# Optimization experiments

Measured on AMD Instinct MI355X. Metric: run time of the kernel, lower is better.

The kernel has to match this reference:

```python
import jax, jax.numpy as jnp
import numpy as np
import math

POOL = 7          # RoIAlign output_size
SR = 2            # sampling_ratio


def _roi_align(feat, boxes, bidx):
    """torchvision RoIAlign, aligned=False, spatial_scale=1.0, sampling_ratio=2.
    feat: [B,C,H,W]; boxes: [N,4] (x1,y1,x2,y2) in pixel coords of this level;
    bidx: [N] int batch indices. Returns [N,C,POOL,POOL]."""
    B, C, H, W = feat.shape
    x1, y1, x2, y2 = boxes[:, 0], boxes[:, 1], boxes[:, 2], boxes[:, 3]
    roi_w = jnp.maximum(x2 - x1, 1.0)
    roi_h = jnp.maximum(y2 - y1, 1.0)
    bin_w = roi_w / POOL
    bin_h = roi_h / POOL
    # sample-point offsets within the ROI, in bin units: [POOL, SR]
    off = jnp.arange(POOL, dtype=feat.dtype)[:, None] + (jnp.arange(SR, dtype=feat.dtype)[None, :] + 0.5) / SR
    ys = y1[:, None, None] + bin_h[:, None, None] * off  # [N,POOL,SR]
    xs = x1[:, None, None] + bin_w[:, None, None] * off  # [N,POOL,SR]

    def prep(c, size):
        valid = (c > -1.0) & (c < size)
        c = jnp.clip(c, 0.0, size - 1)
        lo = jnp.floor(c).astype(jnp.int32)
        hi = jnp.minimum(lo + 1, size - 1)
        return lo, hi, c - lo, valid

    y_lo, y_hi, fy, vy = prep(ys, H)
    x_lo, x_hi, fx, vx = prep(xs, W)

    b = bidx.astype(jnp.int32)[:, None, None, None, None]  # [N,1,1,1,1]

    def gather(yi, xi):
        # -> [N,POOL,SR,POOL,SR,C] (advanced indices broadcast, channel slice last)
        return feat[b, :, yi[:, :, :, None, None], xi[:, None, None, :, :]]

    hy = (1.0 - fy)[:, :, :, None, None, None]
    ly = fy[:, :, :, None, None, None]
    hx = (1.0 - fx)[:, None, None, :, :, None]
    lx = fx[:, None, None, :, :, None]
    v = (gather(y_lo, x_lo) * hy * hx + gather(y_lo, x_hi) * hy * lx
         + gather(y_hi, x_lo) * ly * hx + gather(y_hi, x_hi) * ly * lx)
    valid = (vy[:, :, :, None, None] & vx[:, None, None, :, :])[..., None]
    v = jnp.where(valid, v, 0.0)
    out = v.mean(axis=(2, 4))          # average over SRxSR samples -> [N,POOL,POOL,C]
    return out.transpose(0, 3, 1, 2)   # [N,C,POOL,POOL]


def setup_inputs() -> dict:
    key = jax.random.key(0)
    k2, k3, k4, k5, kxy, kwh, kbi = jax.random.split(key, 7)
    N = 1000
    p2 = jax.random.normal(k2, (2, 256, 256, 256), dtype=jnp.float32)
    p3 = jax.random.normal(k3, (2, 256, 128, 128), dtype=jnp.float32)
    p4 = jax.random.normal(k4, (2, 256, 64, 64), dtype=jnp.float32)
    p5 = jax.random.normal(k5, (2, 256, 32, 32), dtype=jnp.float32)
    xy = jax.random.uniform(kxy, (N, 2), minval=0.0, maxval=0.7)
    wh = jax.random.uniform(kwh, (N, 2), minval=0.02, maxval=0.3)
    rpn_bbox = jnp.concatenate([xy, xy + wh], axis=1)  # (x1,y1,x2,y2) normalized
    box_index = jax.random.randint(kbi, (N,), 0, 2, dtype=jnp.int32)
    return {"p2": p2, "p3": p3, "p4": p4, "p5": p5,
            "rpn_bbox": rpn_bbox, "box_index": box_index}


def reference(p2, p3, p4, p5, rpn_bbox, box_index):
    feats = [p2, p3, p4, p5]
    N = rpn_bbox.shape[0]
    x1, y1, x2, y2 = rpn_bbox[:, 0], rpn_bbox[:, 1], rpn_bbox[:, 2], rpn_bbox[:, 3]
    area = (y2 - y1) * (x2 - x1)
    roi_level = jnp.log(jnp.sqrt(area)) / math.log(2.0)
    roi_level = jnp.clip(jnp.round(roi_level) + 4.0, 0.0, 3.0).astype(jnp.int32)
    # Compute RoIAlign of every ROI at every level, then select per-ROI level.
    # (The masked-select / per-level dispatch / argsort-combine in the original
    # restores original ROI order, so this is mathematically identical.)
    pooled_per_level = jnp.stack(
        [_roi_align(f, rpn_bbox * f.shape[3], box_index) for f in feats], axis=0
    )  # [4, N, C, 7, 7]
    pooled = pooled_per_level[roi_level, jnp.arange(N)]  # [N, C, 7, 7]
    return pooled
```

## Files before the change

### kernel.cpp

```cpp
#include <hip/hip_runtime.h>
#include <math.h>

#define POOL 7
#define NCELL 49
#define NCH 256
#define CH_SPLIT 4
#define CHPB (NCH / CH_SPLIT)
#define CHPW (CHPB / 4)
#define LDSF 640
#define NIT 10

__global__ __launch_bounds__(256) void roi_align_fpn_kernel(
    const float* __restrict__ p2, const float* __restrict__ p3,
    const float* __restrict__ p4, const float* __restrict__ p5,
    const float* __restrict__ boxes, const int* __restrict__ bidx,
    float* __restrict__ out, int N)
{
    __shared__ float smem[4][LDSF];
    const int n = blockIdx.x;
    if (n >= N) return;
    const int t = threadIdx.x;
    const int wave = t >> 6;
    const int lane = t & 63;

    float bx1 = boxes[4 * n + 0], by1 = boxes[4 * n + 1];
    float bx2 = boxes[4 * n + 2], by2 = boxes[4 * n + 3];
    float area = (by2 - by1) * (bx2 - bx1);
    float lvlf = logf(sqrtf(area)) * 1.4426950408889634f;
    int level = (int)fminf(fmaxf(rintf(lvlf) + 4.0f, 0.0f), 3.0f);
    int W = 256 >> level;
    int HW = W * W;
    float scale = (float)W;
    float x1 = bx1 * scale, y1 = by1 * scale;
    float bin_w = fmaxf((bx2 - bx1) * scale, 1.0f) * (1.0f / POOL);
    float bin_h = fmaxf((by2 - by1) * scale, 1.0f) * (1.0f / POOL);

    const float* feat = (level == 0) ? p2 : (level == 1) ? p3 : (level == 2) ? p4 : p5;
    feat += (size_t)bidx[n] * NCH * HW;

    float yA = y1 + bin_h * 0.25f, yB = y1 + bin_h * 6.75f;
    float xA = x1 + bin_w * 0.25f, xB = x1 + bin_w * 6.75f;
    int y0  = (int)floorf(fminf(fmaxf(yA, 0.f), (float)(W - 1)));
    int y1h = min((int)floorf(fminf(fmaxf(yB, 0.f), (float)(W - 1))) + 1, W - 1);
    int x0  = (int)floorf(fminf(fmaxf(xA, 0.f), (float)(W - 1)));
    x0 = min(x0, W - 2);
    int x1p = min((int)floorf(fminf(fmaxf(xB, 0.f), (float)(W - 1))) + 1, W - 1);
    int ww = x1p - x0 + 1;
    int wh = y1h - y0 + 1;
    wh = min(wh, LDSF / ww);
    int packed = ww * wh;

    int g_off[NIT];
#pragma unroll
    for (int k = 0; k < NIT; ++k) {
        int idx = k * 64 + lane;
        idx = (idx < packed) ? idx : 0;
        int r = idx / ww;
        int c = idx - r * ww;
        g_off[k] = (y0 + r) * W + (x0 + c);
    }

    int cell = (lane < NCELL) ? lane : (NCELL - 1);
    int py = cell / POOL, px = cell % POOL;
    int loff0[4], loff1[4];
    float w00[4], w01[4], w10[4], w11[4];
#pragma unroll
    for (int s = 0; s < 4; ++s) {
        int sy = s >> 1, sx = s & 1;
        float y = y1 + bin_h * ((float)py + ((float)sy + 0.5f) * 0.5f);
        float x = x1 + bin_w * ((float)px + ((float)sx + 0.5f) * 0.5f);
        bool v = (y > -1.f) && (y < (float)W) && (x > -1.f) && (x < (float)W);
        float yc = fminf(fmaxf(y, 0.f), (float)(W - 1));
        float xc = fminf(fmaxf(x, 0.f), (float)(W - 1));
        int ylo = (int)floorf(yc), xlo = (int)floorf(xc);
        int yhi = min(ylo + 1, W - 1);
        float fy = yc - (float)ylo, fx = xc - (float)xlo;
        float vv = v ? 0.25f : 0.f;
        int bxp = min(xlo, W - 2);
        bool in = (xlo == bxp);
        float wx0 = in ? (1.f - fx) : 0.f;
        float wx1 = in ? fx : 1.f;
        float wr0 = (1.f - fy) * vv, wr1 = fy * vv;
        loff0[s] = (ylo - y0) * ww + (bxp - x0);
        loff1[s] = (yhi - y0) * ww + (bxp - x0);
        w00[s] = wr0 * wx0; w01[s] = wr0 * wx1;
        w10[s] = wr1 * wx0; w11[s] = wr1 * wx1;
    }

    float* sm = smem[wave];
    const int ch0 = blockIdx.y * CHPB + wave * CHPW;
    const float* f = feat + (size_t)ch0 * HW;
    size_t obase = (size_t)n * NCH * NCELL + (size_t)ch0 * NCELL + cell;
#pragma unroll 2
    for (int i = 0; i < CHPW; ++i) {
        const float* fc = f + (size_t)i * HW;
        float g[NIT];
#pragma unroll
        for (int k = 0; k < NIT; ++k) g[k] = fc[g_off[k]];
#pragma unroll
        for (int k = 0; k < NIT; ++k) sm[k * 64 + lane] = g[k];
        float acc = 0.f;
#pragma unroll
        for (int s = 0; s < 4; ++s) {
            float a0 = sm[loff0[s]], a1 = sm[loff0[s] + 1];
            float b0 = sm[loff1[s]], b1 = sm[loff1[s] + 1];
            acc += w00[s] * a0 + w01[s] * a1 + w10[s] * b0 + w11[s] * b1;
        }
        if (lane < NCELL)
            __builtin_nontemporal_store(acc, out + obase + (size_t)i * NCELL);
    }
}

extern "C" void kernel_launch(void* const* d_in, const int* in_sizes, int n_in,
                              void* d_out, int out_size, void* d_ws, size_t ws_size,
                              hipStream_t stream) {
    const float* p2    = (const float*)d_in[0];
    const float* p3    = (const float*)d_in[1];
    const float* p4    = (const float*)d_in[2];
    const float* p5    = (const float*)d_in[3];
    const float* boxes = (const float*)d_in[4];
    const int*   bidx  = (const int*)d_in[5];
    float* out = (float*)d_out;
    int N = in_sizes[5];
    dim3 grid(N, CH_SPLIT);
    roi_align_fpn_kernel<<<grid, 256, 0, stream>>>(p2, p3, p4, p5, boxes, bidx, out, N);
}
```

Measured before the change: 286.3 us.

## Double-buffer feature patches via async global-to-LDS loads and reorder grid

Replaces register-staged gathers with global_load_lds async copies into a double-buffered per-wave LDS region, prefetching the next channel's patch while the current one is interpolated. It doubles the channel split and swaps the grid axes so that blocks for the same ROI launch adjacently, which should improve L2 locality, and it raises the launch-bounds occupancy hint. The goal is to hide gather latency and cut register traffic. In exchange it relies on manual vmcnt waits, doubles LDS use per block, and drops the N bounds check.

```diff
diff --git a/kernel.cpp b/kernel.cpp
--- a/kernel.cpp
+++ b/kernel.cpp
@@ -4,21 +4,26 @@
 #define POOL 7
 #define NCELL 49
 #define NCH 256
-#define CH_SPLIT 4
+#define CH_SPLIT 8
 #define CHPB (NCH / CH_SPLIT)
 #define CHPW (CHPB / 4)
 #define LDSF 640
 #define NIT 10
 
-__global__ __launch_bounds__(256) void roi_align_fpn_kernel(
+typedef __attribute__((address_space(1))) void global_void;
+typedef __attribute__((address_space(3))) void lds_void;
+__device__ __forceinline__ void async_stage(const float* g, float* l) {
+    __builtin_amdgcn_global_load_lds((global_void*)g, (lds_void*)l, 4, 0, 0);
+}
+
+__global__ __launch_bounds__(256, 8) void roi_align_fpn_kernel(
     const float* __restrict__ p2, const float* __restrict__ p3,
     const float* __restrict__ p4, const float* __restrict__ p5,
     const float* __restrict__ boxes, const int* __restrict__ bidx,
     float* __restrict__ out, int N)
 {
-    __shared__ float smem[4][LDSF];
-    const int n = blockIdx.x;
-    if (n >= N) return;
+    __shared__ float smem[4][2][LDSF];
+    const int n = blockIdx.y;
     const int t = threadIdx.x;
     const int wave = t >> 6;
     const int lane = t & 63;
@@ -60,6 +65,13 @@
         g_off[k] = (y0 + r) * W + (x0 + c);
     }
 
+    const int ch0 = blockIdx.x * CHPB + wave * CHPW;
+    const float* fbase = feat + (size_t)ch0 * HW;
+    float* sm = &smem[wave][0][0];
+
+#pragma unroll
+    for (int k = 0; k < NIT; ++k) async_stage(fbase + g_off[k], sm + k * 64);
+
     int cell = (lane < NCELL) ? lane : (NCELL - 1);
     int py = cell / POOL, px = cell % POOL;
     int loff0[4], loff1[4];
@@ -87,23 +99,24 @@
         w10[s] = wr1 * wx0; w11[s] = wr1 * wx1;
     }
 
-    float* sm = smem[wave];
-    const int ch0 = blockIdx.y * CHPB + wave * CHPW;
-    const float* f = feat + (size_t)ch0 * HW;
     size_t obase = (size_t)n * NCH * NCELL + (size_t)ch0 * NCELL + cell;
-#pragma unroll 2
+#pragma unroll
     for (int i = 0; i < CHPW; ++i) {
-        const float* fc = f + (size_t)i * HW;
-        float g[NIT];
+        if (i + 1 < CHPW) {
+            const float* fc = fbase + (size_t)(i + 1) * HW;
+            float* nb = sm + ((i + 1) & 1) * LDSF;
 #pragma unroll
-        for (int k = 0; k < NIT; ++k) g[k] = fc[g_off[k]];
-#pragma unroll
-        for (int k = 0; k < NIT; ++k) sm[k * 64 + lane] = g[k];
+            for (int k = 0; k < NIT; ++k) async_stage(fc + g_off[k], nb + k * 64);
+            asm volatile("s_waitcnt vmcnt(10)" ::: "memory");
+        } else {
+            asm volatile("s_waitcnt vmcnt(0)" ::: "memory");
+        }
+        const float* cb = sm + (i & 1) * LDSF;
         float acc = 0.f;
 #pragma unroll
         for (int s = 0; s < 4; ++s) {
-            float a0 = sm[loff0[s]], a1 = sm[loff0[s] + 1];
-            float b0 = sm[loff1[s]], b1 = sm[loff1[s] + 1];
+            float a0 = cb[loff0[s]], a1 = cb[loff0[s] + 1];
+            float b0 = cb[loff1[s]], b1 = cb[loff1[s] + 1];
             acc += w00[s] * a0 + w01[s] * a1 + w10[s] * b0 + w11[s] * b1;
         }
         if (lane < NCELL)
@@ -122,6 +135,6 @@
     const int*   bidx  = (const int*)d_in[5];
     float* out = (float*)d_out;
     int N = in_sizes[5];
-    dim3 grid(N, CH_SPLIT);
+    dim3 grid(CH_SPLIT, N);
     roi_align_fpn_kernel<<<grid, 256, 0, stream>>>(p2, p3, p4, p5, boxes, bidx, out, N);
 }
```

Measured after the change: 274.3 us. 1.04x faster.
